# Performance work log

Measured on AMD Instinct MI355X. Metric: run time of the kernel, lower is better.

The kernel has to match this reference:

```python
import jax, jax.numpy as jnp
import numpy as np

MARGIN = 0.3
EPS = 1e-6      # torch F.pairwise_distance eps used inside TripletMarginLoss
BIG = 1000000.0  # same sentinel as original code


def setup_inputs() -> dict:
    key = jax.random.key(0)
    k1, k2 = jax.random.split(key)
    embeddings = jax.random.normal(k1, (4096, 2048), dtype=jnp.float32)
    labels = jax.random.randint(k2, (4096,), 0, 128)  # 128 identities -> ~32 samples each
    return {"embeddings": embeddings, "labels": labels}


def _batch_hard_triplet_loss(emb, labels):
    B = emb.shape[0]
    # pairwise euclidean distances (torch.cdist p=2)
    sq = jnp.sum(emb * emb, axis=1)                      # [B]
    d2 = sq[:, None] + sq[None, :] - 2.0 * (emb @ emb.T)  # [B,B]
    dists = jnp.sqrt(jnp.maximum(d2, 0.0))

    same = labels[:, None] == labels[None, :]            # [B,B] bool
    eye = jnp.eye(B, dtype=bool)
    pos_mask = same & ~eye

    # hard positive: argmax over same-label (self set to -1, others-with-diff-label masked to 0*d -> use -1 uniformly for non-positives, matching dists*mask_pos with diag=-1 since dists>=0)
    pos_d = jnp.where(pos_mask, dists, -1.0)
    hard_pos = jnp.argmax(pos_d, axis=1)                 # [B]
    # hard negative: argmin over different-label (same-label gets +1e6 like original)
    neg_d = jnp.where(same, dists + BIG, dists)
    hard_neg = jnp.argmin(neg_d, axis=1)                 # [B]

    # valid anchors: at least one positive (other than self) and one negative
    valid = (jnp.sum(pos_mask, axis=1) > 0) & (jnp.sum(~same, axis=1) > 0)

    # TripletMarginLoss recomputes distances with eps added to the difference
    dp = jnp.linalg.norm(emb - emb[hard_pos] + EPS, axis=1)
    dn = jnp.linalg.norm(emb - emb[hard_neg] + EPS, axis=1)
    per = jnp.maximum(dp - dn + MARGIN, 0.0)

    cnt = jnp.sum(valid)
    total = jnp.sum(jnp.where(valid, per, 0.0))
    return jnp.where(cnt > 0, total / jnp.maximum(cnt, 1).astype(per.dtype), 0.0)


def reference(embeddings, labels):
    return _batch_hard_triplet_loss(embeddings, labels)
```

## Files before the change

### kernel.cpp

```cpp
#include <hip/hip_runtime.h>
#include <stdint.h>

#define B 4096
#define D 2048
#define BK 128

typedef unsigned long long ull;
typedef float f32x4 __attribute__((ext_vector_type(4)));

#define SENT_P 0x00000000FFFFFFFFull
#define SENT_N (~0ull)

__device__ __forceinline__ void async_copy16(const unsigned char* g, unsigned char* l) {
  __builtin_amdgcn_global_load_lds(
      (const __attribute__((address_space(1))) unsigned int*)g,
      (__attribute__((address_space(3))) unsigned int*)l,
      16, 0, 0);
}

__global__ void k_convert_sq(const float* __restrict__ emb,
                             unsigned char* __restrict__ embq,
                             float* __restrict__ sq,
                             float* __restrict__ rs,
                             ull* __restrict__ bp,
                             ull* __restrict__ bn) {
  const int row = blockIdx.x, t = threadIdx.x;
  const float4* src = (const float4*)(emb + (size_t)row * D);
  float4 v0 = src[2 * t], v1 = src[2 * t + 1];
  float s = v0.x * v0.x + v0.y * v0.y + v0.z * v0.z + v0.w * v0.w
          + v1.x * v1.x + v1.y * v1.y + v1.z * v1.z + v1.w * v1.w;
  float sm = v0.x + v0.y + v0.z + v0.w + v1.x + v1.y + v1.z + v1.w;

  unsigned w0 = __builtin_amdgcn_cvt_pk_fp8_f32(v0.x, v0.y, 0, false);
  w0 = __builtin_amdgcn_cvt_pk_fp8_f32(v0.z, v0.w, w0, true);
  unsigned w1 = __builtin_amdgcn_cvt_pk_fp8_f32(v1.x, v1.y, 0, false);
  w1 = __builtin_amdgcn_cvt_pk_fp8_f32(v1.z, v1.w, w1, true);
  uint2 o; o.x = w0; o.y = w1;
  ((uint2*)(embq + (size_t)row * D))[t] = o;

  for (int off = 32; off; off >>= 1) {
    s  += __shfl_down(s, off, 64);
    sm += __shfl_down(sm, off, 64);
  }
  __shared__ float ps[4], pm[4];
  int lane = t & 63, wave = t >> 6;
  if (lane == 0) { ps[wave] = s; pm[wave] = sm; }
  __syncthreads();
  if (t == 0) {
    sq[row] = ps[0] + ps[1] + ps[2] + ps[3];
    rs[row] = pm[0] + pm[1] + pm[2] + pm[3];
    bp[row] = SENT_P;
    bn[row] = SENT_N;
  }
}

__launch_bounds__(128, 3)
__global__ void k_gemm_select(const unsigned char* __restrict__ embq,
                              const float* __restrict__ sq,
                              const int* __restrict__ labels,
                              ull* __restrict__ best_pos,
                              ull* __restrict__ best_neg) {
  __shared__ unsigned char ldsA[64 * BK];
  __shared__ unsigned char ldsB[128 * BK];

  int rem = blockIdx.x, p = 0;
  while (rem >= 2 * (32 - p)) { rem -= 2 * (32 - p); ++p; }
  int by = 2 * p;
  int c = 32 - p;
  if (rem >= c) { by += 1; rem -= c; }
  const int bx = p + rem;

  const int tid  = threadIdx.x;
  const int lane = tid & 63;
  const int wave = tid >> 6;
  const int wn = wave;
  const int q = lane >> 4, m15 = lane & 15;
  const int ibase = by * 64, jbase = bx * 128;

  int aoff[4][4], boff[4][4];
#pragma unroll
  for (int s = 0; s < 4; ++s) {
#pragma unroll
    for (int xg = 0; xg < 4; ++xg) {
      int rowA = xg * 16 + m15;
      aoff[s][xg] = rowA * BK + (((s * 2 + (q >> 1)) ^ (rowA & 7)) * 16) + (q & 1) * 8;
      int rowB = wn * 64 + xg * 16 + m15;
      boff[s][xg] = rowB * BK + (((s * 2 + (q >> 1)) ^ (rowB & 7)) * 16) + (q & 1) * 8;
    }
  }

  const int srow = lane >> 3;
  const int slot = lane & 7;

  f32x4 acc[4][4];
  const f32x4 z = {0.f, 0.f, 0.f, 0.f};
#pragma unroll
  for (int a = 0; a < 4; ++a)
#pragma unroll
    for (int b = 0; b < 4; ++b) acc[a][b] = z;

  for (int kb = 0; kb < D; kb += BK) {
    __syncthreads();
#pragma unroll
    for (int pp = 0; pp < 4; ++pp) {
      int r0  = wave * 32 + pp * 8;
      int row = r0 + srow;
      int g   = (slot ^ (row & 7)) * 16;
      const unsigned char* ga = embq + (size_t)(ibase + row) * D + kb + g;
      async_copy16(ga, &ldsA[r0 * BK]);
    }
#pragma unroll
    for (int pp = 0; pp < 8; ++pp) {
      int r0  = wave * 64 + pp * 8;
      int row = r0 + srow;
      int g   = (slot ^ (row & 7)) * 16;
      const unsigned char* gb = embq + (size_t)(jbase + row) * D + kb + g;
      async_copy16(gb, &ldsB[r0 * BK]);
    }
    __syncthreads();

#pragma unroll
    for (int s = 0; s < 4; ++s) {
      long af[4];
      long bfr[4];
#pragma unroll
      for (int xg = 0; xg < 4; ++xg) af[xg] = *(const long*)&ldsA[aoff[s][xg]];
#pragma unroll
      for (int xg = 0; xg < 4; ++xg) bfr[xg] = *(const long*)&ldsB[boff[s][xg]];
#pragma unroll
      for (int mi = 0; mi < 4; ++mi)
#pragma unroll
        for (int ni = 0; ni < 4; ++ni)
          acc[mi][ni] = __builtin_amdgcn_mfma_f32_16x16x32_fp8_fp8(
              af[mi], bfr[ni], acc[mi][ni], 0, 0, 0);
    }
  }

  float sqj[4];
  int labj[4];
#pragma unroll
  for (int ni = 0; ni < 4; ++ni) {
    int jj = jbase + wn * 64 + ni * 16 + m15;
    sqj[ni] = sq[jj];
    labj[ni] = labels[jj];
  }

  ull colBp[4], colBn[4];
#pragma unroll
  for (int ni = 0; ni < 4; ++ni) { colBp[ni] = SENT_P; colBn[ni] = SENT_N; }

#pragma unroll
  for (int mi = 0; mi < 4; ++mi) {
#pragma unroll
    for (int r = 0; r < 4; ++r) {
      const int i = ibase + mi * 16 + q * 4 + r;
      const float si = sq[i];
      const int li = labels[i];
      ull bp = SENT_P;
      ull bn = SENT_N;
#pragma unroll
      for (int ni = 0; ni < 4; ++ni) {
        int jj = jbase + wn * 64 + ni * 16 + m15;
        if (jj > i) {
          float dot = acc[mi][ni][r];
          float d2 = si + sqj[ni] - 2.0f * dot;
          float dist = sqrtf(fmaxf(d2, 0.0f));
          ull pv = ((ull)__float_as_uint(dist)) << 32;
          if (labj[ni] == li) {
            ull cr = pv | (unsigned)(~jj);
            bp = bp > cr ? bp : cr;
            ull cc = pv | (unsigned)(~i);
            colBp[ni] = colBp[ni] > cc ? colBp[ni] : cc;
          } else {
            ull cr = pv | (unsigned)jj;
            bn = bn < cr ? bn : cr;
            ull cc = pv | (unsigned)i;
            colBn[ni] = colBn[ni] < cc ? colBn[ni] : cc;
          }
        }
      }
#pragma unroll
      for (int off = 1; off <= 8; off <<= 1) {
        ull op = __shfl_xor(bp, off, 64);
        ull on = __shfl_xor(bn, off, 64);
        bp = bp > op ? bp : op;
        bn = bn < on ? bn : on;
      }
      if (m15 == 0) {
        if (bp != SENT_P) atomicMax(&best_pos[i], bp);
        if (bn != SENT_N) atomicMin(&best_neg[i], bn);
      }
    }
  }

#pragma unroll
  for (int ni = 0; ni < 4; ++ni) {
    ull cp = colBp[ni], cn = colBn[ni];
#pragma unroll
    for (int off = 16; off <= 32; off <<= 1) {
      ull op = __shfl_xor(cp, off, 64);
      ull on = __shfl_xor(cn, off, 64);
      cp = cp > op ? cp : op;
      cn = cn < on ? cn : on;
    }
    if (q == 0) {
      int j = jbase + wn * 64 + ni * 16 + m15;
      if (cp != SENT_P) atomicMax(&best_pos[j], cp);
      if (cn != SENT_N) atomicMin(&best_neg[j], cn);
    }
  }
}

__global__ void k_loss_final(const ull* __restrict__ best_pos,
                             const ull* __restrict__ best_neg,
                             const float* __restrict__ rs,
                             float* __restrict__ out) {
  float per = 0.0f;
  int v = 0;
  for (int i = threadIdx.x; i < B; i += 1024) {
    ull bp = best_pos[i], bn = best_neg[i];
    if (bp != SENT_P && bn != SENT_N) {
      unsigned pRaw = ~(unsigned)bp;
      unsigned nRaw = (unsigned)bn;
      int pi = pRaw < (unsigned)B ? (int)pRaw : 0;
      int ni = nRaw < (unsigned)B ? (int)nRaw : 0;
      float distp = __uint_as_float((unsigned)(bp >> 32));
      float distn = __uint_as_float((unsigned)(bn >> 32));
      float ri = rs[i];
      const float e = 1e-6f, de2 = (float)D * 1e-12f;
      float dp2 = distp * distp + 2.0f * e * (ri - rs[pi]) + de2;
      float dn2 = distn * distn + 2.0f * e * (ri - rs[ni]) + de2;
      float dp = sqrtf(fmaxf(dp2, 0.0f));
      float dn = sqrtf(fmaxf(dn2, 0.0f));
      per += fmaxf(dp - dn + 0.3f, 0.0f);
      v += 1;
    }
  }
  for (int off = 32; off; off >>= 1) {
    per += __shfl_down(per, off, 64);
    v   += __shfl_down(v, off, 64);
  }
  __shared__ float pps[16];
  __shared__ int pvs[16];
  int lane = threadIdx.x & 63, wave = threadIdx.x >> 6;
  if (lane == 0) { pps[wave] = per; pvs[wave] = v; }
  __syncthreads();
  if (threadIdx.x == 0) {
    float t = 0.f;
    int cv = 0;
#pragma unroll
    for (int w = 0; w < 16; ++w) { t += pps[w]; cv += pvs[w]; }
    out[0] = cv > 0 ? t / (float)cv : 0.0f;
  }
}

extern "C" void kernel_launch(void* const* d_in, const int* in_sizes, int n_in,
                              void* d_out, int out_size, void* d_ws, size_t ws_size,
                              hipStream_t stream) {
  const float* emb = (const float*)d_in[0];
  const int* labels = (const int*)d_in[1];
  float* out = (float*)d_out;
  char* ws = (char*)d_ws;

  const size_t off_embq = 0;
  const size_t off_sq   = off_embq + (size_t)B * D;
  const size_t off_rs   = off_sq + (size_t)B * 4;
  const size_t off_bp   = off_rs + (size_t)B * 4;
  const size_t off_bn   = off_bp + (size_t)B * 8;

  unsigned char* embq = (unsigned char*)(ws + off_embq);
  float* sq   = (float*)(ws + off_sq);
  float* rs   = (float*)(ws + off_rs);
  ull* bp     = (ull*)(ws + off_bp);
  ull* bn     = (ull*)(ws + off_bn);

  hipLaunchKernelGGL(k_convert_sq, dim3(B), dim3(256), 0, stream,
                     emb, embq, sq, rs, bp, bn);
  hipLaunchKernelGGL(k_gemm_select, dim3(1056), dim3(128), 0, stream,
                     embq, sq, labels, bp, bn);
  hipLaunchKernelGGL(k_loss_final, dim3(1), dim3(1024), 0, stream,
                     bp, bn, rs, out);
}
```

Before: 131.6 us.

## Register-prefetch next K tile instead of direct global-to-LDS loads

Replaces the direct global_load_lds async copies with a register-staged software pipeline. The next K tile is loaded into registers while MFMAs run on the current LDS tile, then written to LDS at the top of the next iteration. Global and LDS addresses are also precomputed once outside the loop. This aims to hide global load latency behind compute, but costs extra VGPRs (12 uint4) and explicit LDS store instructions, which may reduce occupancy.

```diff
diff --git a/kernel.cpp b/kernel.cpp
--- a/kernel.cpp
+++ b/kernel.cpp
@@ -10,13 +10,6 @@
 
 #define SENT_P 0x00000000FFFFFFFFull
 #define SENT_N (~0ull)
-
-__device__ __forceinline__ void async_copy16(const unsigned char* g, unsigned char* l) {
-  __builtin_amdgcn_global_load_lds(
-      (const __attribute__((address_space(1))) unsigned int*)g,
-      (__attribute__((address_space(3))) unsigned int*)l,
-      16, 0, 0);
-}
 
 __global__ void k_convert_sq(const float* __restrict__ emb,
                              unsigned char* __restrict__ embq,
@@ -92,6 +85,26 @@
   const int srow = lane >> 3;
   const int slot = lane & 7;
 
+  const unsigned char* gA[4];
+  const unsigned char* gB[8];
+  int lA[4], lB[8];
+#pragma unroll
+  for (int pp = 0; pp < 4; ++pp) {
+    int r0  = wave * 32 + pp * 8;
+    int row = r0 + srow;
+    int g   = (slot ^ (row & 7)) * 16;
+    gA[pp] = embq + (size_t)(ibase + row) * D + g;
+    lA[pp] = r0 * BK + (lane << 4);
+  }
+#pragma unroll
+  for (int pp = 0; pp < 8; ++pp) {
+    int r0  = wave * 64 + pp * 8;
+    int row = r0 + srow;
+    int g   = (slot ^ (row & 7)) * 16;
+    gB[pp] = embq + (size_t)(jbase + row) * D + g;
+    lB[pp] = r0 * BK + (lane << 4);
+  }
+
   f32x4 acc[4][4];
   const f32x4 z = {0.f, 0.f, 0.f, 0.f};
 #pragma unroll
@@ -99,25 +112,26 @@
 #pragma unroll
     for (int b = 0; b < 4; ++b) acc[a][b] = z;
 
+  uint4 rA[4], rB[8];
+#pragma unroll
+  for (int pp = 0; pp < 4; ++pp) rA[pp] = *(const uint4*)(gA[pp]);
+#pragma unroll
+  for (int pp = 0; pp < 8; ++pp) rB[pp] = *(const uint4*)(gB[pp]);
+
   for (int kb = 0; kb < D; kb += BK) {
     __syncthreads();
 #pragma unroll
-    for (int pp = 0; pp < 4; ++pp) {
-      int r0  = wave * 32 + pp * 8;
-      int row = r0 + srow;
-      int g   = (slot ^ (row & 7)) * 16;
-      const unsigned char* ga = embq + (size_t)(ibase + row) * D + kb + g;
-      async_copy16(ga, &ldsA[r0 * BK]);
-    }
-#pragma unroll
-    for (int pp = 0; pp < 8; ++pp) {
-      int r0  = wave * 64 + pp * 8;
-      int row = r0 + srow;
-      int g   = (slot ^ (row & 7)) * 16;
-      const unsigned char* gb = embq + (size_t)(jbase + row) * D + kb + g;
-      async_copy16(gb, &ldsB[r0 * BK]);
-    }
+    for (int pp = 0; pp < 4; ++pp) *(uint4*)&ldsA[lA[pp]] = rA[pp];
+#pragma unroll
+    for (int pp = 0; pp < 8; ++pp) *(uint4*)&ldsB[lB[pp]] = rB[pp];
     __syncthreads();
+
+    if (kb + BK < D) {
+#pragma unroll
+      for (int pp = 0; pp < 4; ++pp) rA[pp] = *(const uint4*)(gA[pp] + kb + BK);
+#pragma unroll
+      for (int pp = 0; pp < 8; ++pp) rB[pp] = *(const uint4*)(gB[pp] + kb + BK);
+    }
 
 #pragma unroll
     for (int s = 0; s < 4; ++s) {
```

Result: slower. 239.0 us (+81.6%).
